# Kernel tuning notes

Hardware: AMD Instinct MI355X
Metric: run time of the kernel (lower is better)

Reference implementation:

```python
import jax, jax.numpy as jnp
import numpy as np

N, E, D_IN, D_EDGE = 50000, 800000, 128, 3


def setup_inputs() -> dict:
    key = jax.random.key(0)
    ks = jax.random.split(key, 24)
    p = lambda k, shape, s=0.1: (jax.random.normal(k, shape) * s).astype(jnp.float32)
    return {
        "x": jax.random.normal(ks[0], (N, D_IN), jnp.float32),
        "edge_index": jax.random.randint(ks[1], (2, E), 0, N, dtype=jnp.int32),
        "edge_attr": jax.random.normal(ks[2], (E, D_EDGE), jnp.float32),
        # layer 1: in=128, heads=4, out=64
        "W1": p(ks[3], (D_IN, 256)), "a_src1": p(ks[4], (4, 64)), "a_dst1": p(ks[5], (4, 64)),
        "We1": p(ks[6], (D_EDGE, 256)), "a_e1": p(ks[7], (4, 64)), "b1": jnp.zeros(256, jnp.float32),
        # layer 2: in=256, heads=2, out=32
        "W2": p(ks[8], (256, 64)), "a_src2": p(ks[9], (2, 32)), "a_dst2": p(ks[10], (2, 32)),
        "We2": p(ks[11], (D_EDGE, 64)), "a_e2": p(ks[12], (2, 32)), "b2": jnp.zeros(64, jnp.float32),
        # layer 3: in=64, heads=1, out=16
        "W3": p(ks[13], (64, 16)), "a_src3": p(ks[14], (1, 16)), "a_dst3": p(ks[15], (1, 16)),
        "We3": p(ks[16], (D_EDGE, 16)), "a_e3": p(ks[17], (1, 16)), "b3": jnp.zeros(16, jnp.float32),
    }


def _add_self_loops(src, dst, eattr, n):
    # PyG add_self_loops(fill_value='mean'): loop edge_attr = mean of incoming edge_attr per node
    deg = jax.ops.segment_sum(jnp.ones(src.shape[0], eattr.dtype), dst, num_segments=n)
    mean_attr = jax.ops.segment_sum(eattr, dst, num_segments=n) / jnp.maximum(deg, 1.0)[:, None]
    loop = jnp.arange(n, dtype=src.dtype)
    return (jnp.concatenate([src, loop]), jnp.concatenate([dst, loop]),
            jnp.concatenate([eattr, mean_attr], axis=0))


def _gat_layer(x, src, dst, eattr, W, a_src, a_dst, We, a_e, b):
    H, Oc = a_src.shape
    n = x.shape[0]
    xp = (x @ W).reshape(n, H, Oc)              # [N,H,O] projected nodes
    ep = (eattr @ We).reshape(-1, H, Oc)        # [E,H,O] projected edge attrs
    alpha = ((xp * a_src).sum(-1)[src]          # [E,H] attention logits
             + (xp * a_dst).sum(-1)[dst]
             + (ep * a_e).sum(-1))
    alpha = jnp.where(alpha > 0, alpha, 0.2 * alpha)  # LeakyReLU(0.2)
    m = jax.ops.segment_max(alpha, dst, num_segments=n)  # per-dst softmax (stable)
    ea = jnp.exp(alpha - m[dst])
    att = ea / jax.ops.segment_sum(ea, dst, num_segments=n)[dst]
    agg = jax.ops.segment_sum(xp[src] * att[:, :, None], dst, num_segments=n)
    return agg.reshape(n, H * Oc) + b


def reference(x, edge_index, edge_attr,
              W1, a_src1, a_dst1, We1, a_e1, b1,
              W2, a_src2, a_dst2, We2, a_e2, b2,
              W3, a_src3, a_dst3, We3, a_e3, b3):
    n = x.shape[0]
    src, dst, ea = _add_self_loops(edge_index[0], edge_index[1], edge_attr, n)
    h = jax.nn.elu(_gat_layer(x, src, dst, ea, W1, a_src1, a_dst1, We1, a_e1, b1))
    h = jax.nn.elu(_gat_layer(h, src, dst, ea, W2, a_src2, a_dst2, We2, a_e2, b2))
    return _gat_layer(h, src, dst, ea, W3, a_src3, a_dst3, We3, a_e3, b3)
```

## Files before the change

kernel.cpp:

```cpp
#include <hip/hip_runtime.h>


constexpr int NN  = 50000;
constexpr int NE  = 800000;
constexpr int NET = NE + NN;

typedef __attribute__((ext_vector_type(8))) short bf16x8;
typedef __attribute__((ext_vector_type(4))) float f32x4;

static __device__ __forceinline__ unsigned short f2bf(float f) {
  unsigned u = __float_as_uint(f);
  unsigned r = (u + 0x7FFFu + ((u >> 16) & 1u)) >> 16;
  return (unsigned short)r;
}
static __device__ __forceinline__ float bf2f(unsigned short b) {
  return __uint_as_float((unsigned)b << 16);
}


__global__ __launch_bounds__(256) void k_count(const int* __restrict__ ei,
                                               int* __restrict__ cnt) {
  int e = blockIdx.x * 256 + threadIdx.x;
  if (e >= NE) return;
  atomicAdd(&cnt[ei[NE + e]], 1);
}

__global__ __launch_bounds__(256) void k_scan1(const int* __restrict__ cnt,
                                               int* __restrict__ bsum) {
  __shared__ int lds[256];
  int base = blockIdx.x * 1024;
  int s = 0;
  for (int i = 0; i < 4; i++) {
    int idx = base + threadIdx.x * 4 + i;
    if (idx < NN) s += cnt[idx] + 1;
  }
  lds[threadIdx.x] = s;
  __syncthreads();
  for (int off = 128; off > 0; off >>= 1) {
    if (threadIdx.x < off) lds[threadIdx.x] += lds[threadIdx.x + off];
    __syncthreads();
  }
  if (threadIdx.x == 0) bsum[blockIdx.x] = lds[0];
}

__global__ void k_scan2(int* bsum, int nblk) {
  int run = 0;
  for (int i = 0; i < nblk; i++) { int v = bsum[i]; bsum[i] = run; run += v; }
}

__global__ __launch_bounds__(256) void k_scan3(const int* __restrict__ cnt,
                                               const int* __restrict__ bsum,
                                               int* __restrict__ rowp,
                                               int* __restrict__ cursor) {
  __shared__ int lds[256];
  int t = threadIdx.x;
  int base = blockIdx.x * 1024;
  int v[4];
  int s = 0;
  for (int i = 0; i < 4; i++) {
    int idx = base + t * 4 + i;
    v[i] = (idx < NN) ? cnt[idx] + 1 : 0;
    s += v[i];
  }
  lds[t] = s;
  __syncthreads();
  for (int off = 1; off < 256; off <<= 1) {
    int add = (t >= off) ? lds[t - off] : 0;
    __syncthreads();
    lds[t] += add;
    __syncthreads();
  }
  int p = bsum[blockIdx.x] + lds[t] - s;
  for (int i = 0; i < 4; i++) {
    int idx = base + t * 4 + i;
    if (idx < NN) { rowp[idx] = p; cursor[idx] = p; }
    p += v[i];
  }
  if (blockIdx.x == 0 && t == 0) rowp[NN] = NET;
}

__global__ __launch_bounds__(256) void k_scatter(const int* __restrict__ ei,
                                                 const float* __restrict__ ea,
                                                 int* __restrict__ cursor,
                                                 int4* __restrict__ sorted) {
  int e = blockIdx.x * 256 + threadIdx.x;
  if (e >= NE) return;
  int s = ei[e];
  int d = ei[NE + e];
  int pos = atomicAdd(&cursor[d], 1);
  int4 r;
  r.x = s;
  r.y = __float_as_int(ea[3 * (size_t)e + 0]);
  r.z = __float_as_int(ea[3 * (size_t)e + 1]);
  r.w = __float_as_int(ea[3 * (size_t)e + 2]);
  sorted[pos] = r;
}

__global__ __launch_bounds__(256) void k_segloop(const int* __restrict__ rowp,
                                                 int4* __restrict__ sorted) {
  int t = threadIdx.x, g = t >> 4, gl = t & 15;
  int n = blockIdx.x * 16 + g;
  if (n >= NN) return;
  int rp0 = rowp[n], rp1e = rowp[n + 1] - 1;
  float s0 = 0.f, s1 = 0.f, s2 = 0.f;
  for (int j = rp0 + gl; j < rp1e; j += 16) {
    int4 r = sorted[j];
    s0 += __int_as_float(r.y);
    s1 += __int_as_float(r.z);
    s2 += __int_as_float(r.w);
  }
#pragma unroll
  for (int off = 8; off > 0; off >>= 1) {
    s0 += __shfl_xor(s0, off);
    s1 += __shfl_xor(s1, off);
    s2 += __shfl_xor(s2, off);
  }
  if (gl == 0) {
    float inv = 1.f / fmaxf((float)(rp1e - rp0), 1.f);
    int4 r;
    r.x = n;
    r.y = __float_as_int(s0 * inv);
    r.z = __float_as_int(s1 * inv);
    r.w = __float_as_int(s2 * inv);
    sorted[rp1e] = r;
  }
}

__global__ void k_ce_all(const float* __restrict__ We1, const float* __restrict__ ae1,
                         const float* __restrict__ We2, const float* __restrict__ ae2,
                         const float* __restrict__ We3, const float* __restrict__ ae3,
                         float* __restrict__ ce) {
  int t = threadIdx.x;
  if (t < 12) {
    int d = t / 4, h = t % 4;
    float s = 0.f;
    for (int o = 0; o < 64; o++) s += We1[d * 256 + h * 64 + o] * ae1[h * 64 + o];
    ce[t] = s;
  } else if (t >= 16 && t < 22) {
    int u = t - 16, d = u / 2, h = u % 2;
    float s = 0.f;
    for (int o = 0; o < 32; o++) s += We2[d * 64 + h * 32 + o] * ae2[h * 32 + o];
    ce[t] = s;
  } else if (t >= 24 && t < 27) {
    int d = t - 24;
    float s = 0.f;
    for (int o = 0; o < 16; o++) s += We3[d * 16 + o] * ae3[o];
    ce[t] = s;
  }
}

template <int K, int BN, int O, bool AFP32>
__global__ __launch_bounds__(256) void k_gemm_sc(const void* __restrict__ Ap,
                                                 const float* __restrict__ W,
                                                 unsigned short* __restrict__ Cb,
                                                 const float* __restrict__ a_src,
                                                 const float* __restrict__ a_dst,
                                                 float* __restrict__ ssrc,
                                                 float* __restrict__ sdst,
                                                 int M, int NC) {
  constexpr int NT = BN / 16;
  constexpr int HL = BN / O;
  __shared__ unsigned short Wt[BN][K + 8];
  const int t = threadIdx.x;
  const int row0 = blockIdx.x * 64;
  const int col0 = blockIdx.y * BN;
  const int H = NC / O;
  for (int idx = t; idx < BN * K; idx += 256) {
    int c = idx % BN;
    int k = idx / BN;
    Wt[c][k] = f2bf(W[(size_t)k * NC + col0 + c]);
  }
  __syncthreads();
  const int wave = t >> 6, lane = t & 63;
  const int wc = lane & 15;
  const int rbase = row0 + wave * 16 + wc;
  const int kgrp = (lane >> 4) * 8;
  const bool rok = rbase < M;
  f32x4 acc[NT];
#pragma unroll
  for (int i = 0; i < NT; i++) acc[i] = f32x4{0.f, 0.f, 0.f, 0.f};
#pragma unroll
  for (int kk = 0; kk < K; kk += 32) {
    bf16x8 a = {};
    if (rok) {
      if constexpr (AFP32) {
        const float* Af = (const float*)Ap;
        float4 v0 = *(const float4*)(Af + (size_t)rbase * K + kk + kgrp);
        float4 v1 = *(const float4*)(Af + (size_t)rbase * K + kk + kgrp + 4);
        a[0] = (short)f2bf(v0.x); a[1] = (short)f2bf(v0.y);
        a[2] = (short)f2bf(v0.z); a[3] = (short)f2bf(v0.w);
        a[4] = (short)f2bf(v1.x); a[5] = (short)f2bf(v1.y);
        a[6] = (short)f2bf(v1.z); a[7] = (short)f2bf(v1.w);
      } else {
        a = *(const bf16x8*)((const unsigned short*)Ap + (size_t)rbase * K + kk + kgrp);
      }
    }
#pragma unroll
    for (int nt = 0; nt < NT; nt++) {
      bf16x8 b = *(const bf16x8*)(&Wt[nt * 16 + wc][kk + kgrp]);
      acc[nt] = __builtin_amdgcn_mfma_f32_16x16x32_bf16(a, b, acc[nt], 0, 0, 0);
    }
  }
  const int wr0 = row0 + wave * 16 + (lane >> 4) * 4;
  float psrc[4][HL], pdst[4][HL];
#pragma unroll
  for (int i = 0; i < 4; i++)
#pragma unroll
    for (int hl = 0; hl < HL; hl++) { psrc[i][hl] = 0.f; pdst[i][hl] = 0.f; }
#pragma unroll
  for (int nt = 0; nt < NT; nt++) {
    const int col = col0 + nt * 16 + wc;
    const float asv = a_src[col];
    const float adv = a_dst[col];
    constexpr int dummy = 0; (void)dummy;
    const int hl = (nt * 16) / O;
#pragma unroll
    for (int i = 0; i < 4; i++) {
      int r = wr0 + i;
      float v = acc[nt][i];
      if (r < M) Cb[(size_t)r * NC + col] = f2bf(v);
      psrc[i][hl] += v * asv;
      pdst[i][hl] += v * adv;
    }
  }
#pragma unroll
  for (int off = 1; off < 16; off <<= 1)
#pragma unroll
    for (int i = 0; i < 4; i++)
#pragma unroll
      for (int hl = 0; hl < HL; hl++) {
        psrc[i][hl] += __shfl_xor(psrc[i][hl], off);
        pdst[i][hl] += __shfl_xor(pdst[i][hl], off);
      }
  if (wc == 0) {
#pragma unroll
    for (int i = 0; i < 4; i++) {
      int r = wr0 + i;
      if (r < M) {
#pragma unroll
        for (int hl = 0; hl < HL; hl++) {
          int h = col0 / O + hl;
          ssrc[r * H + h] = psrc[i][hl];
          sdst[r * H + h] = pdst[i][hl];
        }
      }
    }
  }
}

template <int H, int V, bool DO_ELU, bool OB16>
__global__ __launch_bounds__(256) void k_agg2(const int4* __restrict__ sorted,
                                              const int* __restrict__ rowp,
                                              const unsigned short* __restrict__ xpb,
                                              const float* __restrict__ ssrc,
                                              const float* __restrict__ sdst,
                                              const float* __restrict__ ce,
                                              const float* __restrict__ bias,
                                              void* __restrict__ out) {
  constexpr int HO = 64 * V;
  constexpr int OC = HO / H;
  __shared__ float lds_p[4][64][H];
  __shared__ int lds_s[4][64];
  const int wave = threadIdx.x >> 6, lane = threadIdx.x & 63;
  const int n = blockIdx.x * 4 + wave;
  if (n >= NN) return;
  const int rp0 = rowp[n], rp1 = rowp[n + 1];
  const int h_lane = (lane * V) / OC;

  float sd[H], c0[H], c1[H], c2[H];
#pragma unroll
  for (int h = 0; h < H; h++) {
    sd[h] = sdst[n * H + h];
    c0[h] = ce[h];
    c1[h] = ce[H + h];
    c2[h] = ce[2 * H + h];
  }

  float den[H];
#pragma unroll
  for (int h = 0; h < H; h++) den[h] = 0.f;
  float acc[V];
#pragma unroll
  for (int i = 0; i < V; i++) acc[i] = 0.f;

  for (int cbase = rp0; cbase < rp1; cbase += 64) {
    const int cnt = min(64, rp1 - cbase);
    if (lane < cnt) {
      int4 r = sorted[cbase + lane];
      int s = r.x;
      float e0 = __int_as_float(r.y), e1 = __int_as_float(r.z), e2 = __int_as_float(r.w);
      float sv[H];
      if constexpr (H == 4) {
        float4 v = *(const float4*)(ssrc + 4 * (size_t)s);
        sv[0] = v.x; sv[1] = v.y; sv[2] = v.z; sv[3] = v.w;
      } else if constexpr (H == 2) {
        float2 v = *(const float2*)(ssrc + 2 * (size_t)s);
        sv[0] = v.x; sv[1] = v.y;
      } else {
        sv[0] = ssrc[s];
      }
#pragma unroll
      for (int h = 0; h < H; h++) {
        float a = sv[h] + sd[h] + e0 * c0[h] + e1 * c1[h] + e2 * c2[h];
        a = a > 0.f ? a : 0.2f * a;
        float p = __expf(a);
        den[h] += p;
        lds_p[wave][lane][h] = p;
      }
      lds_s[wave][lane] = s;
    }
    for (int c = 0; c < cnt; c++) {
      const float pw = lds_p[wave][c][h_lane];
      const int s = lds_s[wave][c];
      const unsigned short* row = xpb + (size_t)s * HO + lane * V;
      if constexpr (V == 4) {
        ushort4 u = *(const ushort4*)row;
        acc[0] += pw * bf2f(u.x);
        acc[1] += pw * bf2f(u.y);
        acc[2] += pw * bf2f(u.z);
        acc[3] += pw * bf2f(u.w);
      } else {
        acc[0] += pw * bf2f(row[0]);
      }
    }
  }
#pragma unroll
  for (int off = 32; off > 0; off >>= 1)
#pragma unroll
    for (int h = 0; h < H; h++) den[h] += __shfl_xor(den[h], off);

  const float dinv = 1.f / den[h_lane];
#pragma unroll
  for (int i = 0; i < V; i++) {
    const int jc = lane * V + i;
    float v = acc[i] * dinv + bias[jc];
    if constexpr (DO_ELU) v = v > 0.f ? v : __expf(v) - 1.f;
    if constexpr (OB16) {
      ((unsigned short*)out)[(size_t)n * HO + jc] = f2bf(v);
    } else {
      ((float*)out)[(size_t)n * HO + jc] = v;
    }
  }
}

__global__ __launch_bounds__(256) void k_agg3(const int4* __restrict__ sorted,
                                              const int* __restrict__ rowp,
                                              const unsigned short* __restrict__ xpb,
                                              const float* __restrict__ ssrc,
                                              const float* __restrict__ sdst,
                                              const float* __restrict__ ce,
                                              const float* __restrict__ bias,
                                              float* __restrict__ out) {
  __shared__ float lds_p[16][16];
  __shared__ int lds_s[16][16];
  int t = threadIdx.x, g = t >> 4, gl = t & 15;
  int n = blockIdx.x * 16 + g;
  if (n >= NN) return;
  int rp0 = rowp[n], rp1 = rowp[n + 1];
  float sd = sdst[n], ce0 = ce[0], ce1 = ce[1], ce2 = ce[2];

  float den = 0.f, acc = 0.f;
  for (int cbase = rp0; cbase < rp1; cbase += 16) {
    int cnt = min(16, rp1 - cbase);
    if (gl < cnt) {
      int4 r = sorted[cbase + gl];
      float a = ssrc[r.x] + sd + __int_as_float(r.y) * ce0 +
                __int_as_float(r.z) * ce1 + __int_as_float(r.w) * ce2;
      a = a > 0.f ? a : 0.2f * a;
      float p = __expf(a);
      den += p;
      lds_p[g][gl] = p;
      lds_s[g][gl] = r.x;
    }
    for (int c = 0; c < cnt; c++)
      acc += lds_p[g][c] * bf2f(xpb[(size_t)lds_s[g][c] * 16 + gl]);
  }
#pragma unroll
  for (int off = 8; off > 0; off >>= 1) den += __shfl_xor(den, off);
  out[(size_t)n * 16 + gl] = acc / den + bias[gl];
}


extern "C" void kernel_launch(void* const* d_in, const int* in_sizes, int n_in,
                              void* d_out, int out_size, void* d_ws, size_t ws_size,
                              hipStream_t stream) {
  const float* x   = (const float*)d_in[0];
  const int*   ei  = (const int*)d_in[1];
  const float* ea  = (const float*)d_in[2];
  const float* W1  = (const float*)d_in[3];
  const float* as1 = (const float*)d_in[4];
  const float* ad1 = (const float*)d_in[5];
  const float* We1 = (const float*)d_in[6];
  const float* ae1 = (const float*)d_in[7];
  const float* b1  = (const float*)d_in[8];
  const float* W2  = (const float*)d_in[9];
  const float* as2 = (const float*)d_in[10];
  const float* ad2 = (const float*)d_in[11];
  const float* We2 = (const float*)d_in[12];
  const float* ae2 = (const float*)d_in[13];
  const float* b2  = (const float*)d_in[14];
  const float* W3  = (const float*)d_in[15];
  const float* as3 = (const float*)d_in[16];
  const float* ad3 = (const float*)d_in[17];
  const float* We3 = (const float*)d_in[18];
  const float* ae3 = (const float*)d_in[19];
  const float* b3  = (const float*)d_in[20];
  float* out = (float*)d_out;

  char* base = (char*)d_ws;
  size_t off = 0;
  auto get = [&](size_t bytes) -> char* {
    char* q = base + off;
    off += (bytes + 255) & ~(size_t)255;
    return q;
  };
  int*   cnt    = (int*)get((size_t)NN * 4);
  int*   rowp   = (int*)get((size_t)(NN + 1) * 4);
  int*   cursor = (int*)get((size_t)NN * 4);
  int*   bsum   = (int*)get(256 * 4);
  int4*  sorted = (int4*)get((size_t)NET * 16);
  float* ssrc   = (float*)get((size_t)NN * 16);
  float* sdst   = (float*)get((size_t)NN * 16);
  float* ce     = (float*)get(256);
  unsigned short* xb  = (unsigned short*)get((size_t)NN * 256 * 2);
  unsigned short* h1b = (unsigned short*)get((size_t)NN * 256 * 2);
  unsigned short* h2b = (unsigned short*)get((size_t)NN * 64 * 2);
  (void)ws_size; (void)in_sizes; (void)n_in; (void)out_size;

  hipMemsetAsync(cnt, 0, (size_t)NN * 4, stream);

  const int EB = (NE + 255) / 256;
  const int SB = (NN + 1023) / 1024;

  k_count<<<EB, 256, 0, stream>>>(ei, cnt);
  k_scan1<<<SB, 256, 0, stream>>>(cnt, bsum);
  k_scan2<<<1, 1, 0, stream>>>(bsum, SB);
  k_scan3<<<SB, 256, 0, stream>>>(cnt, bsum, rowp, cursor);
  k_scatter<<<EB, 256, 0, stream>>>(ei, ea, cursor, sorted);
  k_segloop<<<(NN + 15) / 16, 256, 0, stream>>>(rowp, sorted);
  k_ce_all<<<1, 64, 0, stream>>>(We1, ae1, We2, ae2, We3, ae3, ce);

  const int GR64 = (NN + 63) / 64;
  const int AGB = (NN + 3) / 4;

  k_gemm_sc<128, 64, 64, true><<<dim3(GR64, 4), 256, 0, stream>>>(
      (const void*)x, W1, xb, as1, ad1, ssrc, sdst, NN, 256);
  k_agg2<4, 4, true, true><<<AGB, 256, 0, stream>>>(sorted, rowp, xb, ssrc, sdst, ce, b1, (void*)h1b);

  k_gemm_sc<256, 64, 32, false><<<dim3(GR64, 1), 256, 0, stream>>>(
      (const void*)h1b, W2, xb, as2, ad2, ssrc, sdst, NN, 64);
  k_agg2<2, 1, true, true><<<AGB, 256, 0, stream>>>(sorted, rowp, xb, ssrc, sdst, ce + 16, b2, (void*)h2b);

  k_gemm_sc<64, 16, 16, false><<<dim3(GR64, 1), 256, 0, stream>>>(
      (const void*)h2b, W3, xb, as3, ad3, ssrc, sdst, NN, 16);
  k_agg3<<<(NN + 15) / 16, 256, 0, stream>>>(sorted, rowp, xb, ssrc, sdst, ce + 24, b3, out);
}
```

Baseline: 392.2 us.

## Record per-edge rank during counting, merge tiny kernels, specialize layer-2 aggregation

The degree-count kernel now stores each edge's atomic rank, so the scatter step becomes an atomic-free placement at rowp[d]+rank[e] instead of a second round of cursor atomics. The serial block-sum scan and the edge-coefficient kernel are merged into one launch. Layer-2 aggregation gets its own kernel in which each wave handles two edges at once, using all 64 lanes on 32-wide feature pairs, where the old version left lanes idle. The trade-off is an extra 3.2MB rank buffer that must be written and read back.

```diff
diff --git a/kernel.cpp b/kernel.cpp
--- a/kernel.cpp
+++ b/kernel.cpp
@@ -18,21 +18,22 @@
 }
 
 
-__global__ __launch_bounds__(256) void k_count(const int* __restrict__ ei,
-                                               int* __restrict__ cnt) {
+__global__ __launch_bounds__(256) void k_rank(const int* __restrict__ ei,
+                                              int* __restrict__ deg,
+                                              int* __restrict__ rank) {
   int e = blockIdx.x * 256 + threadIdx.x;
   if (e >= NE) return;
-  atomicAdd(&cnt[ei[NE + e]], 1);
-}
-
-__global__ __launch_bounds__(256) void k_scan1(const int* __restrict__ cnt,
+  rank[e] = atomicAdd(&deg[ei[NE + e]], 1);
+}
+
+__global__ __launch_bounds__(256) void k_scan1(const int* __restrict__ deg,
                                                int* __restrict__ bsum) {
   __shared__ int lds[256];
   int base = blockIdx.x * 1024;
   int s = 0;
   for (int i = 0; i < 4; i++) {
     int idx = base + threadIdx.x * 4 + i;
-    if (idx < NN) s += cnt[idx] + 1;
+    if (idx < NN) s += deg[idx] + 1;
   }
   lds[threadIdx.x] = s;
   __syncthreads();
@@ -43,95 +44,16 @@
   if (threadIdx.x == 0) bsum[blockIdx.x] = lds[0];
 }
 
-__global__ void k_scan2(int* bsum, int nblk) {
-  int run = 0;
-  for (int i = 0; i < nblk; i++) { int v = bsum[i]; bsum[i] = run; run += v; }
-}
-
-__global__ __launch_bounds__(256) void k_scan3(const int* __restrict__ cnt,
-                                               const int* __restrict__ bsum,
-                                               int* __restrict__ rowp,
-                                               int* __restrict__ cursor) {
-  __shared__ int lds[256];
+__global__ void k_scan2_ce(int* __restrict__ bsum, int nblk,
+                           const float* __restrict__ We1, const float* __restrict__ ae1,
+                           const float* __restrict__ We2, const float* __restrict__ ae2,
+                           const float* __restrict__ We3, const float* __restrict__ ae3,
+                           float* __restrict__ ce) {
   int t = threadIdx.x;
-  int base = blockIdx.x * 1024;
-  int v[4];
-  int s = 0;
-  for (int i = 0; i < 4; i++) {
-    int idx = base + t * 4 + i;
-    v[i] = (idx < NN) ? cnt[idx] + 1 : 0;
-    s += v[i];
-  }
-  lds[t] = s;
-  __syncthreads();
-  for (int off = 1; off < 256; off <<= 1) {
-    int add = (t >= off) ? lds[t - off] : 0;
-    __syncthreads();
-    lds[t] += add;
-    __syncthreads();
-  }
-  int p = bsum[blockIdx.x] + lds[t] - s;
-  for (int i = 0; i < 4; i++) {
-    int idx = base + t * 4 + i;
-    if (idx < NN) { rowp[idx] = p; cursor[idx] = p; }
-    p += v[i];
-  }
-  if (blockIdx.x == 0 && t == 0) rowp[NN] = NET;
-}
-
-__global__ __launch_bounds__(256) void k_scatter(const int* __restrict__ ei,
-                                                 const float* __restrict__ ea,
-                                                 int* __restrict__ cursor,
-                                                 int4* __restrict__ sorted) {
-  int e = blockIdx.x * 256 + threadIdx.x;
-  if (e >= NE) return;
-  int s = ei[e];
-  int d = ei[NE + e];
-  int pos = atomicAdd(&cursor[d], 1);
-  int4 r;
-  r.x = s;
-  r.y = __float_as_int(ea[3 * (size_t)e + 0]);
-  r.z = __float_as_int(ea[3 * (size_t)e + 1]);
-  r.w = __float_as_int(ea[3 * (size_t)e + 2]);
-  sorted[pos] = r;
-}
-
-__global__ __launch_bounds__(256) void k_segloop(const int* __restrict__ rowp,
-                                                 int4* __restrict__ sorted) {
-  int t = threadIdx.x, g = t >> 4, gl = t & 15;
-  int n = blockIdx.x * 16 + g;
-  if (n >= NN) return;
-  int rp0 = rowp[n], rp1e = rowp[n + 1] - 1;
-  float s0 = 0.f, s1 = 0.f, s2 = 0.f;
-  for (int j = rp0 + gl; j < rp1e; j += 16) {
-    int4 r = sorted[j];
-    s0 += __int_as_float(r.y);
-    s1 += __int_as_float(r.z);
-    s2 += __int_as_float(r.w);
-  }
-#pragma unroll
-  for (int off = 8; off > 0; off >>= 1) {
-    s0 += __shfl_xor(s0, off);
-    s1 += __shfl_xor(s1, off);
-    s2 += __shfl_xor(s2, off);
-  }
-  if (gl == 0) {
-    float inv = 1.f / fmaxf((float)(rp1e - rp0), 1.f);
-    int4 r;
-    r.x = n;
-    r.y = __float_as_int(s0 * inv);
-    r.z = __float_as_int(s1 * inv);
-    r.w = __float_as_int(s2 * inv);
-    sorted[rp1e] = r;
-  }
-}
-
-__global__ void k_ce_all(const float* __restrict__ We1, const float* __restrict__ ae1,
-                         const float* __restrict__ We2, const float* __restrict__ ae2,
-                         const float* __restrict__ We3, const float* __restrict__ ae3,
-                         float* __restrict__ ce) {
-  int t = threadIdx.x;
-  if (t < 12) {
+  if (t == 63) {
+    int run = 0;
+    for (int i = 0; i < nblk; i++) { int v = bsum[i]; bsum[i] = run; run += v; }
+  } else if (t < 12) {
     int d = t / 4, h = t % 4;
     float s = 0.f;
     for (int o = 0; o < 64; o++) s += We1[d * 256 + h * 64 + o] * ae1[h * 64 + o];
@@ -146,6 +68,82 @@
     float s = 0.f;
     for (int o = 0; o < 16; o++) s += We3[d * 16 + o] * ae3[o];
     ce[t] = s;
+  }
+}
+
+__global__ __launch_bounds__(256) void k_scan3(const int* __restrict__ deg,
+                                               const int* __restrict__ bsum,
+                                               int* __restrict__ rowp) {
+  __shared__ int lds[256];
+  int t = threadIdx.x;
+  int base = blockIdx.x * 1024;
+  int v[4];
+  int s = 0;
+  for (int i = 0; i < 4; i++) {
+    int idx = base + t * 4 + i;
+    v[i] = (idx < NN) ? deg[idx] + 1 : 0;
+    s += v[i];
+  }
+  lds[t] = s;
+  __syncthreads();
+  for (int off = 1; off < 256; off <<= 1) {
+    int add = (t >= off) ? lds[t - off] : 0;
+    __syncthreads();
+    lds[t] += add;
+    __syncthreads();
+  }
+  int p = bsum[blockIdx.x] + lds[t] - s;
+  for (int i = 0; i < 4; i++) {
+    int idx = base + t * 4 + i;
+    if (idx < NN) rowp[idx] = p;
+    p += v[i];
+  }
+  if (blockIdx.x == 0 && t == 0) rowp[NN] = NET;
+}
+
+__global__ __launch_bounds__(256) void k_place(const int* __restrict__ ei,
+                                               const float* __restrict__ ea,
+                                               const int* __restrict__ rank,
+                                               const int* __restrict__ rowp,
+                                               int4* __restrict__ sorted) {
+  int e = blockIdx.x * 256 + threadIdx.x;
+  if (e >= NE) return;
+  int d = ei[NE + e];
+  int4 r;
+  r.x = ei[e];
+  r.y = __float_as_int(ea[3 * (size_t)e + 0]);
+  r.z = __float_as_int(ea[3 * (size_t)e + 1]);
+  r.w = __float_as_int(ea[3 * (size_t)e + 2]);
+  sorted[rowp[d] + rank[e]] = r;
+}
+
+__global__ __launch_bounds__(256) void k_segloop(const int* __restrict__ rowp,
+                                                 int4* __restrict__ sorted) {
+  int t = threadIdx.x, g = t >> 4, gl = t & 15;
+  int n = blockIdx.x * 16 + g;
+  if (n >= NN) return;
+  int rp0 = rowp[n], rp1e = rowp[n + 1] - 1;
+  float s0 = 0.f, s1 = 0.f, s2 = 0.f;
+  for (int j = rp0 + gl; j < rp1e; j += 16) {
+    int4 r = sorted[j];
+    s0 += __int_as_float(r.y);
+    s1 += __int_as_float(r.z);
+    s2 += __int_as_float(r.w);
+  }
+#pragma unroll
+  for (int off = 8; off > 0; off >>= 1) {
+    s0 += __shfl_xor(s0, off);
+    s1 += __shfl_xor(s1, off);
+    s2 += __shfl_xor(s2, off);
+  }
+  if (gl == 0) {
+    float inv = 1.f / fmaxf((float)(rp1e - rp0), 1.f);
+    int4 r;
+    r.x = n;
+    r.y = __float_as_int(s0 * inv);
+    r.z = __float_as_int(s1 * inv);
+    r.w = __float_as_int(s2 * inv);
+    sorted[rp1e] = r;
   }
 }
 
@@ -212,7 +210,6 @@
     const int col = col0 + nt * 16 + wc;
     const float asv = a_src[col];
     const float adv = a_dst[col];
-    constexpr int dummy = 0; (void)dummy;
     const int hl = (nt * 16) / O;
 #pragma unroll
     for (int i = 0; i < 4; i++) {
@@ -248,24 +245,23 @@
   }
 }
 
-template <int H, int V, bool DO_ELU, bool OB16>
-__global__ __launch_bounds__(256) void k_agg2(const int4* __restrict__ sorted,
-                                              const int* __restrict__ rowp,
-                                              const unsigned short* __restrict__ xpb,
-                                              const float* __restrict__ ssrc,
-                                              const float* __restrict__ sdst,
-                                              const float* __restrict__ ce,
-                                              const float* __restrict__ bias,
-                                              void* __restrict__ out) {
-  constexpr int HO = 64 * V;
-  constexpr int OC = HO / H;
+
+__global__ __launch_bounds__(256) void k_agg_l1(const int4* __restrict__ sorted,
+                                                const int* __restrict__ rowp,
+                                                const unsigned short* __restrict__ xpb,
+                                                const float* __restrict__ ssrc,
+                                                const float* __restrict__ sdst,
+                                                const float* __restrict__ ce,
+                                                const float* __restrict__ bias,
+                                                unsigned short* __restrict__ out) {
+  constexpr int H = 4;
   __shared__ float lds_p[4][64][H];
   __shared__ int lds_s[4][64];
   const int wave = threadIdx.x >> 6, lane = threadIdx.x & 63;
   const int n = blockIdx.x * 4 + wave;
   if (n >= NN) return;
   const int rp0 = rowp[n], rp1 = rowp[n + 1];
-  const int h_lane = (lane * V) / OC;
+  const int h_lane = lane >> 4;
 
   float sd[H], c0[H], c1[H], c2[H];
 #pragma unroll
@@ -276,12 +272,8 @@
     c2[h] = ce[2 * H + h];
   }
 
-  float den[H];
-#pragma unroll
-  for (int h = 0; h < H; h++) den[h] = 0.f;
-  float acc[V];
-#pragma unroll
-  for (int i = 0; i < V; i++) acc[i] = 0.f;
+  float den[H] = {0.f, 0.f, 0.f, 0.f};
+  float acc[4] = {0.f, 0.f, 0.f, 0.f};
 
   for (int cbase = rp0; cbase < rp1; cbase += 64) {
     const int cnt = min(64, rp1 - cbase);
@@ -289,16 +281,8 @@
       int4 r = sorted[cbase + lane];
       int s = r.x;
       float e0 = __int_as_float(r.y), e1 = __int_as_float(r.z), e2 = __int_as_float(r.w);
-      float sv[H];
-      if constexpr (H == 4) {
-        float4 v = *(const float4*)(ssrc + 4 * (size_t)s);
-        sv[0] = v.x; sv[1] = v.y; sv[2] = v.z; sv[3] = v.w;
-      } else if constexpr (H == 2) {
-        float2 v = *(const float2*)(ssrc + 2 * (size_t)s);
-        sv[0] = v.x; sv[1] = v.y;
-      } else {
-        sv[0] = ssrc[s];
-      }
+      float4 v = *(const float4*)(ssrc + 4 * (size_t)s);
+      float sv[H] = {v.x, v.y, v.z, v.w};
 #pragma unroll
       for (int h = 0; h < H; h++) {
         float a = sv[h] + sd[h] + e0 * c0[h] + e1 * c1[h] + e2 * c2[h];
@@ -312,16 +296,11 @@
     for (int c = 0; c < cnt; c++) {
       const float pw = lds_p[wave][c][h_lane];
       const int s = lds_s[wave][c];
-      const unsigned short* row = xpb + (size_t)s * HO + lane * V;
-      if constexpr (V == 4) {
-        ushort4 u = *(const ushort4*)row;
-        acc[0] += pw * bf2f(u.x);
-        acc[1] += pw * bf2f(u.y);
-        acc[2] += pw * bf2f(u.z);
-        acc[3] += pw * bf2f(u.w);
-      } else {
-        acc[0] += pw * bf2f(row[0]);
-      }
+      ushort4 u = *(const ushort4*)(xpb + (size_t)s * 256 + lane * 4);
+      acc[0] += pw * bf2f(u.x);
+      acc[1] += pw * bf2f(u.y);
+      acc[2] += pw * bf2f(u.z);
+      acc[3] += pw * bf2f(u.w);
     }
   }
 #pragma unroll
@@ -331,15 +310,83 @@
 
   const float dinv = 1.f / den[h_lane];
 #pragma unroll
-  for (int i = 0; i < V; i++) {
-    const int jc = lane * V + i;
+  for (int i = 0; i < 4; i++) {
+    const int jc = lane * 4 + i;
     float v = acc[i] * dinv + bias[jc];
-    if constexpr (DO_ELU) v = v > 0.f ? v : __expf(v) - 1.f;
-    if constexpr (OB16) {
-      ((unsigned short*)out)[(size_t)n * HO + jc] = f2bf(v);
-    } else {
-      ((float*)out)[(size_t)n * HO + jc] = v;
-    }
+    v = v > 0.f ? v : __expf(v) - 1.f;
+    out[(size_t)n * 256 + jc] = f2bf(v);
+  }
+}
+
+__global__ __launch_bounds__(256) void k_agg_l2(const int4* __restrict__ sorted,
+                                                const int* __restrict__ rowp,
+                                                const unsigned short* __restrict__ xpb,
+                                                const float* __restrict__ ssrc,
+                                                const float* __restrict__ sdst,
+                                                const float* __restrict__ ce,
+                                                const float* __restrict__ bias,
+                                                unsigned short* __restrict__ out) {
+  __shared__ float lds_p[4][64][2];
+  __shared__ int lds_s[4][64];
+  const int wave = threadIdx.x >> 6, lane = threadIdx.x & 63;
+  const int n = blockIdx.x * 4 + wave;
+  if (n >= NN) return;
+  const int rp0 = rowp[n], rp1 = rowp[n + 1];
+  const int eh = lane >> 5;
+  const int cl = lane & 31;
+  const int h_cl = cl >> 4;
+
+  float sd0 = sdst[n * 2 + 0], sd1 = sdst[n * 2 + 1];
+  float c00 = ce[0], c01 = ce[1], c10 = ce[2], c11 = ce[3], c20 = ce[4], c21 = ce[5];
+
+  float den0 = 0.f, den1 = 0.f;
+  float acc0 = 0.f, acc1 = 0.f;
+
+  for (int cbase = rp0; cbase < rp1; cbase += 64) {
+    const int cnt = min(64, rp1 - cbase);
+    if (lane < cnt) {
+      int4 r = sorted[cbase + lane];
+      int s = r.x;
+      float e0 = __int_as_float(r.y), e1 = __int_as_float(r.z), e2 = __int_as_float(r.w);
+      float2 v = *(const float2*)(ssrc + 2 * (size_t)s);
+      float a0 = v.x + sd0 + e0 * c00 + e1 * c10 + e2 * c20;
+      float a1 = v.y + sd1 + e0 * c01 + e1 * c11 + e2 * c21;
+      a0 = a0 > 0.f ? a0 : 0.2f * a0;
+      a1 = a1 > 0.f ? a1 : 0.2f * a1;
+      float p0 = __expf(a0), p1 = __expf(a1);
+      den0 += p0; den1 += p1;
+      lds_p[wave][lane][0] = p0;
+      lds_p[wave][lane][1] = p1;
+      lds_s[wave][lane] = s;
+    }
+    for (int c = 0; c < cnt; c += 2) {
+      const int e = c + eh;
+      const bool ok = e < cnt;
+      const int ei_ = ok ? e : 0;
+      const float pw = ok ? lds_p[wave][ei_][h_cl] : 0.f;
+      const int s = lds_s[wave][ei_];
+      ushort2 u = *(const ushort2*)(xpb + (size_t)s * 64 + cl * 2);
+      acc0 += pw * bf2f(u.x);
+      acc1 += pw * bf2f(u.y);
+    }
+  }
+  acc0 += __shfl_xor(acc0, 32);
+  acc1 += __shfl_xor(acc1, 32);
+#pragma unroll
+  for (int off = 32; off > 0; off >>= 1) {
+    den0 += __shfl_xor(den0, off);
+    den1 += __shfl_xor(den1, off);
+  }
+  if (eh == 0) {
+    const float dinv = 1.f / (h_cl == 0 ? den0 : den1);
+    const int col = cl * 2;
+    float v0 = acc0 * dinv + bias[col];
+    float v1 = acc1 * dinv + bias[col + 1];
+    v0 = v0 > 0.f ? v0 : __expf(v0) - 1.f;
+    v1 = v1 > 0.f ? v1 : __expf(v1) - 1.f;
+    ushort2 o;
+    o.x = f2bf(v0); o.y = f2bf(v1);
+    *(ushort2*)(out + (size_t)n * 64 + col) = o;
   }
 }
 
@@ -414,9 +461,9 @@
     off += (bytes + 255) & ~(size_t)255;
     return q;
   };
-  int*   cnt    = (int*)get((size_t)NN * 4);
+  int*   deg    = (int*)get((size_t)NN * 4);
+  int*   rank   = (int*)get((size_t)NE * 4);
   int*   rowp   = (int*)get((size_t)(NN + 1) * 4);
-  int*   cursor = (int*)get((size_t)NN * 4);
   int*   bsum   = (int*)get(256 * 4);
   int4*  sorted = (int4*)get((size_t)NET * 16);
   float* ssrc   = (float*)get((size_t)NN * 16);
@@ -427,29 +474,28 @@
   unsigned short* h2b = (unsigned short*)get((size_t)NN * 64 * 2);
   (void)ws_size; (void)in_sizes; (void)n_in; (void)out_size;
 
-  hipMemsetAsync(cnt, 0, (size_t)NN * 4, stream);
+  hipMemsetAsync(deg, 0, (size_t)NN * 4, stream);
 
   const int EB = (NE + 255) / 256;
   const int SB = (NN + 1023) / 1024;
 
-  k_count<<<EB, 256, 0, stream>>>(ei, cnt);
-  k_scan1<<<SB, 256, 0, stream>>>(cnt, bsum);
-  k_scan2<<<1, 1, 0, stream>>>(bsum, SB);
-  k_scan3<<<SB, 256, 0, stream>>>(cnt, bsum, rowp, cursor);
-  k_scatter<<<EB, 256, 0, stream>>>(ei, ea, cursor, sorted);
+  k_rank<<<EB, 256, 0, stream>>>(ei, deg, rank);
+  k_scan1<<<SB, 256, 0, stream>>>(deg, bsum);
+  k_scan2_ce<<<1, 64, 0, stream>>>(bsum, SB, We1, ae1, We2, ae2, We3, ae3, ce);
+  k_scan3<<<SB, 256, 0, stream>>>(deg, bsum, rowp);
+  k_place<<<EB, 256, 0, stream>>>(ei, ea, rank, rowp, sorted);
   k_segloop<<<(NN + 15) / 16, 256, 0, stream>>>(rowp, sorted);
-  k_ce_all<<<1, 64, 0, stream>>>(We1, ae1, We2, ae2, We3, ae3, ce);
 
   const int GR64 = (NN + 63) / 64;
   const int AGB = (NN + 3) / 4;
 
   k_gemm_sc<128, 64, 64, true><<<dim3(GR64, 4), 256, 0, stream>>>(
       (const void*)x, W1, xb, as1, ad1, ssrc, sdst, NN, 256);
-  k_agg2<4, 4, true, true><<<AGB, 256, 0, stream>>>(sorted, rowp, xb, ssrc, sdst, ce, b1, (void*)h1b);
+  k_agg_l1<<<AGB, 256, 0, stream>>>(sorted, rowp, xb, ssrc, sdst, ce, b1, h1b);
 
   k_gemm_sc<256, 64, 32, false><<<dim3(GR64, 1), 256, 0, stream>>>(
       (const void*)h1b, W2, xb, as2, ad2, ssrc, sdst, NN, 64);
-  k_agg2<2, 1, true, true><<<AGB, 256, 0, stream>>>(sorted, rowp, xb, ssrc, sdst, ce + 16, b2, (void*)h2b);
+  k_agg_l2<<<AGB, 256, 0, stream>>>(sorted, rowp, xb, ssrc, sdst, ce + 16, b2, h2b);
 
   k_gemm_sc<64, 16, 16, false><<<dim3(GR64, 1), 256, 0, stream>>>(
       (const void*)h2b, W3, xb, as3, ad3, ssrc, sdst, NN, 16);
```

New measurement: 355.1 us. 9.5% less time.
